# Optimization experiments

Measured on AMD Instinct MI355X. Metric: run time of the kernel, lower is better.

## Reference

```python
import jax, jax.numpy as jnp
import numpy as np

B, NQ, S, H, NH = 2, 1024, 4096, 1024, 16
HD = H // NH
EPS = 1e-6


def layer_norm(x, gamma, beta):
    mu = jnp.mean(x, axis=-1, keepdims=True)
    var = jnp.mean(jnp.square(x - mu), axis=-1, keepdims=True)
    return (x - mu) * jax.lax.rsqrt(var + EPS) * gamma + beta


def setup_inputs() -> dict:
    key = jax.random.key(0)
    ks = jax.random.split(key, 6)
    queries = jax.random.normal(ks[0], (B, NQ, H), dtype=jnp.float32)
    keys_values = jax.random.normal(ks[1], (B, S, H), dtype=jnp.float32)
    attention_mask = jax.random.uniform(ks[2], (B, S)) > 0.1
    attention_mask = attention_mask.at[:, 0].set(True)
    # params (torch Linear stored transposed here so y = x @ W + b)
    W_qkv = jax.random.normal(ks[3], (H, 3 * H), dtype=jnp.float32) * 0.02
    b_qkv = jnp.zeros((3 * H,), dtype=jnp.float32)
    W_out = jax.random.normal(ks[4], (H, H), dtype=jnp.float32) * 0.02
    b_out = jnp.zeros((H,), dtype=jnp.float32)
    gamma = jnp.ones((H,), dtype=jnp.float32)
    beta = jnp.zeros((H,), dtype=jnp.float32)
    return {"queries": queries, "keys_values": keys_values,
            "attention_mask": attention_mask,
            "W_qkv": W_qkv, "b_qkv": b_qkv, "W_out": W_out, "b_out": b_out,
            "gamma": gamma, "beta": beta}


def reference(queries, keys_values, attention_mask, W_qkv, b_qkv, W_out, b_out, gamma, beta):
    # shared LayerNorm + shared qkv projection applied to both streams
    q_in = layer_norm(queries, gamma, beta)
    kv_in = layer_norm(keys_values, gamma, beta)
    q = (q_in @ W_qkv + b_qkv)[..., :H]                    # [B,NQ,H]
    kv = kv_in @ W_qkv + b_qkv
    k = kv[..., H:2 * H]                                    # [B,S,H]
    v = kv[..., 2 * H:]                                     # [B,S,H]
    q = q.reshape(B, NQ, NH, HD)
    k = k.reshape(B, S, NH, HD)
    v = v.reshape(B, S, NH, HD)
    scale = 1.0 / np.sqrt(HD).astype(np.float32)
    scores = jnp.einsum('bqhd,bkhd->bhqk', q, k) * scale    # [B,NH,NQ,S]
    neg_inf = jnp.finfo(scores.dtype).min
    scores = jnp.where(attention_mask[:, None, None, :], scores, neg_inf)
    attn = jax.nn.softmax(scores, axis=-1)
    out = jnp.einsum('bhqk,bkhd->bqhd', attn, v).reshape(B, NQ, H)
    return out @ W_out + b_out
```

## Files before the change

### kernel.cpp

```cpp
#include <hip/hip_runtime.h>
#include <stdint.h>

#define DEVI __device__ __forceinline__

constexpr int Bb = 2, NQ = 1024, S = 4096, H = 1024, NH = 16, HD = 64;
constexpr int NSPLIT = 4, SLEN = S / NSPLIT;

typedef __bf16 bf16x8 __attribute__((ext_vector_type(8)));
typedef float f32x4 __attribute__((ext_vector_type(4)));
typedef int i32x4 __attribute__((ext_vector_type(4)));
typedef unsigned short u16;
typedef u16 u16x8 __attribute__((ext_vector_type(8)));

DEVI u16 f2bf(float f) {
  union { float f; unsigned u; } v; v.f = f;
  unsigned r = (v.u + 0x7fffu + ((v.u >> 16) & 1u)) >> 16;
  return (u16)r;
}

DEVI float bf2f(u16 x) {
  union { unsigned u; float f; } v; v.u = ((unsigned)x) << 16;
  return v.f;
}

DEVI float fexp2(float x) {
#if __has_builtin(__builtin_amdgcn_exp2f)
  return __builtin_amdgcn_exp2f(x);
#else
  return exp2f(x);
#endif
}

DEVI void gload_lds16(const void* g, void* lds) {
  __builtin_amdgcn_global_load_lds(
      (const __attribute__((address_space(1))) void*)(uintptr_t)g,
      (__attribute__((address_space(3))) void*)(uint32_t)(uintptr_t)lds,
      16, 0, 0);
}

DEVI void ln_body(const float* __restrict__ x, const float* __restrict__ gamma,
                  const float* __restrict__ beta, u16* __restrict__ out, int row) {
  int lane = threadIdx.x & 63;
  const float4* xr = (const float4*)(x + (size_t)row * H);
  float4 v[4];
  float s = 0.f, s2 = 0.f;
#pragma unroll
  for (int i = 0; i < 4; ++i) {
    v[i] = xr[lane + i * 64];
    s += v[i].x + v[i].y + v[i].z + v[i].w;
    s2 += v[i].x * v[i].x + v[i].y * v[i].y + v[i].z * v[i].z + v[i].w * v[i].w;
  }
#pragma unroll
  for (int d = 1; d < 64; d <<= 1) { s += __shfl_xor(s, d); s2 += __shfl_xor(s2, d); }
  float mu = s * (1.f / H);
  float rstd = rsqrtf(s2 * (1.f / H) - mu * mu + 1e-6f);
  u16* orow = out + (size_t)row * H;
  const float4* g4 = (const float4*)gamma;
  const float4* b4 = (const float4*)beta;
#pragma unroll
  for (int i = 0; i < 4; ++i) {
    float4 g = g4[lane + i * 64], bb = b4[lane + i * 64];
    ushort4 o;
    o.x = f2bf((v[i].x - mu) * rstd * g.x + bb.x);
    o.y = f2bf((v[i].y - mu) * rstd * g.y + bb.y);
    o.z = f2bf((v[i].z - mu) * rstd * g.z + bb.z);
    o.w = f2bf((v[i].w - mu) * rstd * g.w + bb.w);
    *(ushort4*)(orow + (size_t)(lane + i * 64) * 4) = o;
  }
}

__global__ __launch_bounds__(256) void prep_kernel(
    const unsigned char* __restrict__ mraw, unsigned char* __restrict__ maskN,
    const float* __restrict__ queries, const float* __restrict__ keys_values,
    const float* __restrict__ gamma, const float* __restrict__ beta,
    u16* __restrict__ Xq, u16* __restrict__ Xkv,
    const float* __restrict__ W_qkv, const float* __restrict__ W_out,
    u16* __restrict__ Wtq, u16* __restrict__ Wto) {
  __shared__ int isByte;
  __shared__ float tile[32][33];
  const int b = blockIdx.x;
  if (b == 0) {
    if (threadIdx.x == 0) isByte = 0;
    __syncthreads();
    int any = 0;
    for (int p = threadIdx.x; p < Bb * S; p += 256)
      if ((p & 3) && mraw[p]) any = 1;
    if (any) atomicOr(&isByte, 1);
    __syncthreads();
    const int bytemode = isByte;
    for (int i = threadIdx.x; i < Bb * S; i += 256) {
      unsigned char v = bytemode ? (unsigned char)(mraw[i] != 0)
                                 : (unsigned char)(((const int*)mraw)[i] != 0);
      maskN[i] = v;
    }
  } else if (b < 513) {
    ln_body(queries, gamma, beta, Xq, (b - 1) * 4 + (threadIdx.x >> 6));
  } else if (b < 2561) {
    ln_body(keys_values, gamma, beta, Xkv, (b - 513) * 4 + (threadIdx.x >> 6));
  } else {
    const float* in; u16* out; int C, t;
    if (b < 5633) { t = b - 2561; in = W_qkv; out = Wtq; C = 3 * H; }
    else          { t = b - 5633; in = W_out; out = Wto; C = H; }
    const int nbx = C / 32;
    int c0 = (t % nbx) * 32, r0 = (t / nbx) * 32;
    int tx = threadIdx.x & 31, ty = threadIdx.x >> 5;
#pragma unroll
    for (int i = 0; i < 32; i += 8)
      tile[ty + i][tx] = in[(size_t)(r0 + ty + i) * C + c0 + tx];
    __syncthreads();
#pragma unroll
    for (int i = 0; i < 32; i += 8)
      out[(size_t)(c0 + ty + i) * H + r0 + tx] = f2bf(tile[tx][ty + i]);
  }
}

#define GEMM_CORE(Ag, Bg)                                                        \
  f32x4 acc[4][4] = {};                                                          \
  {                                                                              \
    for (int k0 = 0; k0 < 1024; k0 += 32) {                                      \
      gload_lds16(Ag + (size_t)(c0 >> 2) * 1024 + k0 + (c0 & 3) * 8, Ash + c0 * 8); \
      gload_lds16(Ag + (size_t)(c1 >> 2) * 1024 + k0 + (c1 & 3) * 8, Ash + c1 * 8); \
      gload_lds16(Bg + (size_t)(c0 >> 2) * 1024 + k0 + (c0 & 3) * 8, Bsh + c0 * 8); \
      gload_lds16(Bg + (size_t)(c1 >> 2) * 1024 + k0 + (c1 & 3) * 8, Bsh + c1 * 8); \
      asm volatile("s_waitcnt vmcnt(0)" ::: "memory");                           \
      __syncthreads();                                                           \
      bf16x8 af[4], bfr[4];                                                      \
      _Pragma("unroll") for (int m = 0; m < 4; ++m)                              \
          af[m] = *(const bf16x8*)(Ash + (wr + m * 16 + fr) * 32 + fq * 8);      \
      _Pragma("unroll") for (int n = 0; n < 4; ++n)                              \
          bfr[n] = *(const bf16x8*)(Bsh + (wc + n * 16 + fr) * 32 + fq * 8);     \
      _Pragma("unroll") for (int m = 0; m < 4; ++m)                              \
          _Pragma("unroll") for (int n = 0; n < 4; ++n)                          \
              acc[m][n] = __builtin_amdgcn_mfma_f32_16x16x32_bf16(af[m], bfr[n], acc[m][n], 0, 0, 0); \
      __syncthreads();                                                           \
    }                                                                            \
  }

__global__ __launch_bounds__(512, 2) void gemm_kvq_kernel(
    const u16* __restrict__ Xkv, const u16* __restrict__ Xq,
    const u16* __restrict__ Wtq, const float* __restrict__ b_qkv,
    u16* __restrict__ KVbuf, u16* __restrict__ Qbuf) {
  __shared__ __align__(16) u16 Abuf[4][256 * 32];
  __shared__ __align__(16) u16 Bbuf[4][256 * 32];
  const int tid = threadIdx.x, wid = tid >> 6, lane = tid & 63;
  const int fr = lane & 15, fq = lane >> 4;
  const int wr = (wid >> 2) * 128, wc = (wid & 3) * 64;
  const int bid = blockIdx.x;
  const bool isQ = bid >= 256;
  int by, bx;
  const u16 *Ap, *Bp;
  const float* bias;
  if (!isQ) {
    const int xcd = bid & 7, loc = bid >> 3;
    by = xcd * 4 + (loc & 3); bx = loc >> 2;
    Ap = Xkv; Bp = Wtq + (size_t)H * H; bias = b_qkv + H;
  } else {
    const int t = bid - 256;
    by = t >> 2; bx = t & 3;
    Ap = Xq; Bp = Wtq; bias = b_qkv;
  }
  const u16* Ag = Ap + (size_t)(by * 256) * 1024;
  const u16* Bg = Bp + (size_t)(bx * 256) * 1024;

  f32x4 acc[8][4] = {};

  auto stage = [&](int tt) {
    const int k0 = tt * 32;
    u16* Ad = &Abuf[tt & 3][0];
    u16* Bd = &Bbuf[tt & 3][0];
#pragma unroll
    for (int l = 0; l < 2; ++l) {
      int ci = tid + l * 512;
      int row = ci >> 2, ch = ci & 3;
      int chs = ch ^ ((row >> 1) & 3);
      gload_lds16(Ag + (size_t)row * 1024 + k0 + chs * 8, Ad + ci * 8);
      gload_lds16(Bg + (size_t)row * 1024 + k0 + chs * 8, Bd + ci * 8);
    }
  };

#define KV_ITER(T, VM)                                                          \
  {                                                                             \
    asm volatile("s_waitcnt vmcnt(" #VM ")" ::: "memory");                      \
    __syncthreads();                                                            \
    const u16* Ac = &Abuf[(T) & 3][0];                                          \
    const u16* Bc = &Bbuf[(T) & 3][0];                                          \
    bf16x8 af[8], bfv[4];                                                       \
    _Pragma("unroll") for (int m = 0; m < 8; ++m) {                             \
      int row = wr + m * 16 + fr;                                               \
      af[m] = *(const bf16x8*)(Ac + row * 32 + (fq ^ ((row >> 1) & 3)) * 8);    \
    }                                                                           \
    _Pragma("unroll") for (int n = 0; n < 4; ++n) {                             \
      int row = wc + n * 16 + fr;                                               \
      bfv[n] = *(const bf16x8*)(Bc + row * 32 + (fq ^ ((row >> 1) & 3)) * 8);   \
    }                                                                           \
    if ((T) + 3 < 32) stage((T) + 3);                                           \
    __builtin_amdgcn_s_setprio(1);                                              \
    _Pragma("unroll") for (int m = 0; m < 8; ++m)                               \
      _Pragma("unroll") for (int n = 0; n < 4; ++n)                             \
        acc[m][n] = __builtin_amdgcn_mfma_f32_16x16x32_bf16(af[m], bfv[n], acc[m][n], 0, 0, 0); \
    __builtin_amdgcn_s_setprio(0);                                              \
  }

  stage(0);
  stage(1);
  stage(2);
  for (int t = 0; t < 29; ++t) KV_ITER(t, 8)
  KV_ITER(29, 8)
  KV_ITER(30, 4)
  KV_ITER(31, 0)
#undef KV_ITER

  constexpr float QSCALE = 0.125f * 1.4426950408889634f;
#pragma unroll
  for (int m = 0; m < 8; ++m)
#pragma unroll
    for (int n = 0; n < 4; ++n) {
      const int c = bx * 256 + wc + n * 16 + fr;
      const int r0 = by * 256 + wr + m * 16 + fq * 4;
      const float bv = bias[c];
      if (isQ) {
#pragma unroll
        for (int i = 0; i < 4; ++i) {
          int r = r0 + i;
          Qbuf[((((size_t)(r >> 10)) * NH + (c >> 6)) * NQ + (r & (NQ - 1))) * HD + (c & 63)] =
              f2bf((acc[m][n][i] + bv) * QSCALE);
        }
      } else if (c >= 1024) {
        int bb = r0 >> 12, kv = r0 & (S - 1);
        int cc = c - 1024, head = cc >> 6, d = cc & 63;
        ushort4 o;
        o.x = f2bf(acc[m][n][0] + bv);
        o.y = f2bf(acc[m][n][1] + bv);
        o.z = f2bf(acc[m][n][2] + bv);
        o.w = f2bf(acc[m][n][3] + bv);
        u16* vb = KVbuf + (size_t)Bb * NH * S * HD;
        *(ushort4*)(vb + (((size_t)(bb * NH + head)) * HD + d) * S + kv) = o;
      } else {
#pragma unroll
        for (int i = 0; i < 4; ++i) {
          int r = r0 + i;
          KVbuf[((((size_t)(r >> 12)) * NH + (c >> 6)) * S + (r & (S - 1))) * HD + (c & 63)] =
              f2bf(acc[m][n][i] + bv);
        }
      }
    }
}

__global__ __launch_bounds__(256) void gemm_out_kernel(
    const u16* __restrict__ A, const u16* __restrict__ Bt,
    const float* __restrict__ bias, float* __restrict__ outp) {
  __shared__ __align__(16) u16 Ash[128 * 32];
  __shared__ __align__(16) u16 Bsh[128 * 32];
  const int tid = threadIdx.x, w = tid >> 6, lane = tid & 63;
  const int c0 = tid, c1 = tid + 256;
  const int wr = (w >> 1) * 64, wc = (w & 1) * 64;
  const int fr = lane & 15, fq = lane >> 4;
  const int brow = blockIdx.y * 128, bcol = blockIdx.x * 128;
  const u16* Ag = A + (size_t)brow * 1024;
  const u16* Bg = Bt + (size_t)bcol * 1024;
  GEMM_CORE(Ag, Bg)
#pragma unroll
  for (int m = 0; m < 4; ++m)
#pragma unroll
    for (int n = 0; n < 4; ++n) {
      const int c = bcol + wc + n * 16 + fr;
      const int r0 = brow + wr + m * 16 + fq * 4;
#pragma unroll
      for (int i = 0; i < 4; ++i)
        outp[(size_t)(r0 + i) * H + c] = acc[m][n][i] + bias[c];
    }
}

__global__ __launch_bounds__(512, 4) void attn_kernel(
    const u16* __restrict__ Qb, const u16* __restrict__ Kb,
    const u16* __restrict__ Vt, const unsigned char* __restrict__ mask,
    u16* __restrict__ Opart, float2* __restrict__ ml) {
  __shared__ __align__(16) char smem[66560];
  u16* Ktile = (u16*)smem;
  u16* Vtile = (u16*)(smem + 32768);
  float* Mb = (float*)(smem + 65536);
  const int bflat = blockIdx.x;
  const int r = bflat & 7, idx = bflat >> 3;
  const int q0 = (idx & 3) * 256;
  const int g = (idx >> 2) * 8 + r;
  const int bh = g & 31, z = g >> 5;
  const int b = bh >> 4, kv0 = z * SLEN;
  const int tid = threadIdx.x, w = tid >> 6, lane = tid & 63;
  const int fr = lane & 15, fq = lane >> 4, fr7 = fr & 7;
  const u16* QgA = Qb + ((size_t)bh * NQ + q0 + w * 32) * HD;
  const u16* QgB = QgA + 16 * HD;
  const u16* Kg = Kb + (size_t)bh * S * HD;
  const u16* Vg = Vt + (size_t)bh * HD * S;
  const unsigned char* mg = mask + (size_t)b * S + kv0;

  const int kr0 = tid >> 3, kc0 = (tid & 7) ^ (kr0 & 7);
  const int kr1 = (tid + 512) >> 3, kc1 = ((tid + 512) & 7) ^ (kr1 & 7);
  const int vr0 = tid >> 4, vc0 = (tid & 15) ^ (vr0 & 15);
  const int vr1 = (tid + 512) >> 4, vc1 = ((tid + 512) & 15) ^ (vr1 & 15);

  bf16x8 qfA0 = *(const bf16x8*)(QgA + fr * HD + fq * 8);
  bf16x8 qfA1 = *(const bf16x8*)(QgA + fr * HD + 32 + fq * 8);
  bf16x8 qfB0 = *(const bf16x8*)(QgB + fr * HD + fq * 8);
  bf16x8 qfB1 = *(const bf16x8*)(QgB + fr * HD + 32 + fq * 8);

  const int A0 = ((((fq << 1)) & 3) * 16 + fr) << 2;
  const int A1 = ((((fq << 1) + 1) & 3) * 16 + fr) << 2;
  const bool lofq = (fq < 2);

  f32x4 oaccA[4] = {}, oaccB[4] = {};
  float mrowA = -1e30f, lrowA = 0.f, mrowB = -1e30f, lrowB = 0.f;

  auto stageKV = [&](int buf, int kts) {
    gload_lds16(Kg + (size_t)(kv0 + kts + kr0) * HD + kc0 * 8, Ktile + buf * 8192 + tid * 8);
    gload_lds16(Kg + (size_t)(kv0 + kts + kr1) * HD + kc1 * 8, Ktile + buf * 8192 + (tid + 512) * 8);
    gload_lds16(Vg + (size_t)vr0 * S + kv0 + kts + vc0 * 8, Vtile + buf * 8192 + tid * 8);
    gload_lds16(Vg + (size_t)vr1 * S + kv0 + kts + vc1 * 8, Vtile + buf * 8192 + (tid + 512) * 8);
  };

  auto process = [&](int cur, int h) {
    const u16* Kc = Ktile + cur * 8192 + h * 4096;
    const u16* Vc = Vtile + cur * 8192;
    const float* Mc = Mb + cur * 128 + h * 64;

    float svA[4][4], svB[4][4];
    __builtin_amdgcn_s_setprio(1);
#pragma unroll
    for (int nt = 0; nt < 4; ++nt) {
      const u16* kb2 = Kc + (nt * 16 + fr) * 64;
      bf16x8 k0v = *(const bf16x8*)(kb2 + ((fq) ^ fr7) * 8);
      bf16x8 k1v = *(const bf16x8*)(kb2 + ((4 + fq) ^ fr7) * 8);
      f32x4 tA = {}, tB = {};
      tA = __builtin_amdgcn_mfma_f32_16x16x32_bf16(k0v, qfA0, tA, 0, 0, 0);
      tA = __builtin_amdgcn_mfma_f32_16x16x32_bf16(k1v, qfA1, tA, 0, 0, 0);
      tB = __builtin_amdgcn_mfma_f32_16x16x32_bf16(k0v, qfB0, tB, 0, 0, 0);
      tB = __builtin_amdgcn_mfma_f32_16x16x32_bf16(k1v, qfB1, tB, 0, 0, 0);
      float4 mb = *(const float4*)&Mc[nt * 16 + fq * 4];
      svA[nt][0] = tA[0] + mb.x; svA[nt][1] = tA[1] + mb.y;
      svA[nt][2] = tA[2] + mb.z; svA[nt][3] = tA[3] + mb.w;
      svB[nt][0] = tB[0] + mb.x; svB[nt][1] = tB[1] + mb.y;
      svB[nt][2] = tB[2] + mb.z; svB[nt][3] = tB[3] + mb.w;
    }
    __builtin_amdgcn_s_setprio(0);

    float pmaxA, pmaxB;
    {
      float a0 = fmaxf(fmaxf(svA[0][0], svA[0][1]), fmaxf(svA[0][2], svA[0][3]));
      float a1 = fmaxf(fmaxf(svA[1][0], svA[1][1]), fmaxf(svA[1][2], svA[1][3]));
      float a2 = fmaxf(fmaxf(svA[2][0], svA[2][1]), fmaxf(svA[2][2], svA[2][3]));
      float a3 = fmaxf(fmaxf(svA[3][0], svA[3][1]), fmaxf(svA[3][2], svA[3][3]));
      pmaxA = fmaxf(fmaxf(a0, a1), fmaxf(a2, a3));
      float b0 = fmaxf(fmaxf(svB[0][0], svB[0][1]), fmaxf(svB[0][2], svB[0][3]));
      float b1 = fmaxf(fmaxf(svB[1][0], svB[1][1]), fmaxf(svB[1][2], svB[1][3]));
      float b2 = fmaxf(fmaxf(svB[2][0], svB[2][1]), fmaxf(svB[2][2], svB[2][3]));
      float b3 = fmaxf(fmaxf(svB[3][0], svB[3][1]), fmaxf(svB[3][2], svB[3][3]));
      pmaxB = fmaxf(fmaxf(b0, b1), fmaxf(b2, b3));
    }
    if (__any(pmaxA > mrowA + 12.f)) {
      pmaxA = fmaxf(pmaxA, __shfl_xor(pmaxA, 16));
      pmaxA = fmaxf(pmaxA, __shfl_xor(pmaxA, 32));
      float nm = fmaxf(mrowA, pmaxA);
      float al = fexp2(mrowA - nm);
      mrowA = nm; lrowA *= al;
#pragma unroll
      for (int nt = 0; nt < 4; ++nt)
#pragma unroll
        for (int i = 0; i < 4; ++i) oaccA[nt][i] *= al;
    }
    if (__any(pmaxB > mrowB + 12.f)) {
      pmaxB = fmaxf(pmaxB, __shfl_xor(pmaxB, 16));
      pmaxB = fmaxf(pmaxB, __shfl_xor(pmaxB, 32));
      float nm = fmaxf(mrowB, pmaxB);
      float al = fexp2(mrowB - nm);
      mrowB = nm; lrowB *= al;
#pragma unroll
      for (int nt = 0; nt < 4; ++nt)
#pragma unroll
        for (int i = 0; i < 4; ++i) oaccB[nt][i] *= al;
    }

    float pA[4][4], pB[4][4];
#pragma unroll
    for (int nt = 0; nt < 4; ++nt)
#pragma unroll
      for (int i = 0; i < 4; ++i) {
        pA[nt][i] = fexp2(svA[nt][i] - mrowA);
        pB[nt][i] = fexp2(svB[nt][i] - mrowB);
      }
    {
      float s0 = (pA[0][0] + pA[0][1]) + (pA[0][2] + pA[0][3]);
      float s1 = (pA[1][0] + pA[1][1]) + (pA[1][2] + pA[1][3]);
      float s2 = (pA[2][0] + pA[2][1]) + (pA[2][2] + pA[2][3]);
      float s3 = (pA[3][0] + pA[3][1]) + (pA[3][2] + pA[3][3]);
      lrowA += (s0 + s1) + (s2 + s3);
      float t0 = (pB[0][0] + pB[0][1]) + (pB[0][2] + pB[0][3]);
      float t1 = (pB[1][0] + pB[1][1]) + (pB[1][2] + pB[1][3]);
      float t2 = (pB[2][0] + pB[2][1]) + (pB[2][2] + pB[2][3]);
      float t3 = (pB[3][0] + pB[3][1]) + (pB[3][2] + pB[3][3]);
      lrowB += (t0 + t1) + (t2 + t3);
    }

    int pkA[4][2], pkB[4][2];
#pragma unroll
    for (int nt = 0; nt < 4; ++nt) {
      asm("v_cvt_pk_bf16_f32 %0, %1, %2" : "=v"(pkA[nt][0]) : "v"(pA[nt][0]), "v"(pA[nt][1]));
      asm("v_cvt_pk_bf16_f32 %0, %1, %2" : "=v"(pkA[nt][1]) : "v"(pA[nt][2]), "v"(pA[nt][3]));
      asm("v_cvt_pk_bf16_f32 %0, %1, %2" : "=v"(pkB[nt][0]) : "v"(pB[nt][0]), "v"(pB[nt][1]));
      asm("v_cvt_pk_bf16_f32 %0, %1, %2" : "=v"(pkB[nt][1]) : "v"(pB[nt][2]), "v"(pB[nt][3]));
    }

#pragma unroll
    for (int b2 = 0; b2 < 2; ++b2) {
      i32x4 wvA, wvB;
      {
        int w0a = __builtin_amdgcn_ds_bpermute(A0, pkA[2 * b2][0]);
        int w0b = __builtin_amdgcn_ds_bpermute(A0, pkA[2 * b2 + 1][0]);
        int w1a = __builtin_amdgcn_ds_bpermute(A0, pkA[2 * b2][1]);
        int w1b = __builtin_amdgcn_ds_bpermute(A0, pkA[2 * b2 + 1][1]);
        int w2a = __builtin_amdgcn_ds_bpermute(A1, pkA[2 * b2][0]);
        int w2b = __builtin_amdgcn_ds_bpermute(A1, pkA[2 * b2 + 1][0]);
        int w3a = __builtin_amdgcn_ds_bpermute(A1, pkA[2 * b2][1]);
        int w3b = __builtin_amdgcn_ds_bpermute(A1, pkA[2 * b2 + 1][1]);
        wvA[0] = lofq ? w0a : w0b;
        wvA[1] = lofq ? w1a : w1b;
        wvA[2] = lofq ? w2a : w2b;
        wvA[3] = lofq ? w3a : w3b;
      }
      {
        int w0a = __builtin_amdgcn_ds_bpermute(A0, pkB[2 * b2][0]);
        int w0b = __builtin_amdgcn_ds_bpermute(A0, pkB[2 * b2 + 1][0]);
        int w1a = __builtin_amdgcn_ds_bpermute(A0, pkB[2 * b2][1]);
        int w1b = __builtin_amdgcn_ds_bpermute(A0, pkB[2 * b2 + 1][1]);
        int w2a = __builtin_amdgcn_ds_bpermute(A1, pkB[2 * b2][0]);
        int w2b = __builtin_amdgcn_ds_bpermute(A1, pkB[2 * b2 + 1][0]);
        int w3a = __builtin_amdgcn_ds_bpermute(A1, pkB[2 * b2][1]);
        int w3b = __builtin_amdgcn_ds_bpermute(A1, pkB[2 * b2 + 1][1]);
        wvB[0] = lofq ? w0a : w0b;
        wvB[1] = lofq ? w1a : w1b;
        wvB[2] = lofq ? w2a : w2b;
        wvB[3] = lofq ? w3a : w3b;
      }
      bf16x8 pfragA = __builtin_bit_cast(bf16x8, wvA);
      bf16x8 pfragB = __builtin_bit_cast(bf16x8, wvB);
      __builtin_amdgcn_s_setprio(1);
#pragma unroll
      for (int nt = 0; nt < 4; ++nt) {
        const u16* vb2 = Vc + (nt * 16 + fr) * 128;
        bf16x8 vf = *(const bf16x8*)(vb2 + ((h * 8 + b2 * 4 + fq) ^ fr) * 8);
        oaccA[nt] = __builtin_amdgcn_mfma_f32_16x16x32_bf16(vf, pfragA, oaccA[nt], 0, 0, 0);
        oaccB[nt] = __builtin_amdgcn_mfma_f32_16x16x32_bf16(vf, pfragB, oaccB[nt], 0, 0, 0);
      }
      __builtin_amdgcn_s_setprio(0);
    }
  };

  if (tid < 128) Mb[tid] = mg[tid] ? 0.f : -1e30f;
  stageKV(0, 0);
  asm volatile("s_waitcnt vmcnt(0)" ::: "memory");
  __syncthreads();

  int cur = 0;
  for (int kt = 0; kt < SLEN; kt += 128) {
    const int nb = cur ^ 1, kn = kt + 128;
    if (kn < SLEN) {
      if (tid < 128) Mb[nb * 128 + tid] = mg[kn + tid] ? 0.f : -1e30f;
      stageKV(nb, kn);
    }
    process(cur, 0);
    process(cur, 1);
    asm volatile("s_waitcnt vmcnt(0)" ::: "memory");
    __syncthreads();
    cur = nb;
  }

  lrowA += __shfl_xor(lrowA, 16);
  lrowA += __shfl_xor(lrowA, 32);
  lrowB += __shfl_xor(lrowB, 16);
  lrowB += __shfl_xor(lrowB, 32);
  if (fq == 0) {
    ml[((size_t)z * 32 + bh) * NQ + q0 + w * 32 + fr] = float2{mrowA, lrowA};
    ml[((size_t)z * 32 + bh) * NQ + q0 + w * 32 + 16 + fr] = float2{mrowB, lrowB};
  }

  float* tb = (float*)smem + w * 1088;
  const int qloc = lane >> 2, dl = lane & 3;
#pragma unroll
  for (int gsel = 0; gsel < 2; ++gsel) {
    const f32x4* oc = gsel ? oaccB : oaccA;
#pragma unroll
    for (int nt = 0; nt < 4; ++nt)
#pragma unroll
      for (int i = 0; i < 4; ++i)
        tb[fr * 68 + nt * 16 + fq * 4 + i] = oc[nt][i];
    const float* trow = tb + qloc * 68 + dl * 16;
    u16* gdst = Opart +
        (((size_t)z * 32 + bh) * NQ + q0 + w * 32 + gsel * 16 + qloc) * 64 + dl * 16;
    u16x8 o0, o1;
#pragma unroll
    for (int j = 0; j < 8; ++j) {
      o0[j] = f2bf(trow[j]);
      o1[j] = f2bf(trow[8 + j]);
    }
    *(u16x8*)gdst = o0;
    *(u16x8*)(gdst + 8) = o1;
  }
}

__global__ __launch_bounds__(256) void combine_kernel(
    const u16* __restrict__ Opart, const float2* __restrict__ ml,
    u16* __restrict__ out) {
  const int bh = blockIdx.y, b = bh >> 4, h = bh & 15;
  const int q = blockIdx.x * 64 + (threadIdx.x >> 2);
  const int dl = threadIdx.x & 3;
  float2 mm[NSPLIT];
  float M = -1e30f;
#pragma unroll
  for (int zz = 0; zz < NSPLIT; ++zz) {
    mm[zz] = ml[((size_t)zz * 32 + bh) * NQ + q];
    M = fmaxf(M, mm[zz].x);
  }
  float wz[NSPLIT], lsum = 0.f;
#pragma unroll
  for (int zz = 0; zz < NSPLIT; ++zz) {
    wz[zz] = fexp2(mm[zz].x - M);
    lsum += mm[zz].y * wz[zz];
  }
  const float inv = 1.f / lsum;
  float acc[16] = {};
#pragma unroll
  for (int zz = 0; zz < NSPLIT; ++zz) {
    const u16* op = Opart + (((size_t)zz * 32 + bh) * NQ + q) * 64 + dl * 16;
    u16x8 a0 = *(const u16x8*)op;
    u16x8 a1 = *(const u16x8*)(op + 8);
    float wi = wz[zz] * inv;
#pragma unroll
    for (int j = 0; j < 8; ++j) {
      acc[j] += wi * bf2f(a0[j]);
      acc[8 + j] += wi * bf2f(a1[j]);
    }
  }
  u16* orow = out + ((size_t)b * NQ + q) * H + h * HD + dl * 16;
  u16x8 o0, o1;
#pragma unroll
  for (int j = 0; j < 8; ++j) {
    o0[j] = f2bf(acc[j]);
    o1[j] = f2bf(acc[8 + j]);
  }
  *(u16x8*)orow = o0;
  *(u16x8*)(orow + 8) = o1;
}

extern "C" void kernel_launch(void* const* d_in, const int* in_sizes, int n_in,
                              void* d_out, int out_size, void* d_ws, size_t ws_size,
                              hipStream_t stream) {
  const float* queries = (const float*)d_in[0];
  const float* keys_values = (const float*)d_in[1];
  const void* amask = d_in[2];
  const float* W_qkv = (const float*)d_in[3];
  const float* b_qkv = (const float*)d_in[4];
  const float* W_out = (const float*)d_in[5];
  const float* b_out = (const float*)d_in[6];
  const float* gamma = (const float*)d_in[7];
  const float* beta = (const float*)d_in[8];

  char* ws = (char*)d_ws;
  unsigned char* maskN = (unsigned char*)ws;
  u16* Xq = (u16*)(ws + 8192);
  u16* Xkv = Xq + (size_t)Bb * NQ * H;
  u16* Wtq = Xkv + (size_t)Bb * S * H;
  u16* Wto = Wtq + (size_t)3 * H * H;
  u16* Qbuf = Wto + (size_t)H * H;
  u16* Kbuf = Qbuf + (size_t)Bb * NQ * H;
  u16* Aout = Kbuf + (size_t)2 * Bb * S * H;
  u16* Opart = (u16*)(ws + 8192);
  float2* ml = (float2*)((char*)Opart + (size_t)NSPLIT * 32 * NQ * 64 * 2);

  hipLaunchKernelGGL(prep_kernel, dim3(6657), dim3(256), 0, stream,
                     (const unsigned char*)amask, maskN, queries, keys_values,
                     gamma, beta, Xq, Xkv, W_qkv, W_out, Wtq, Wto);
  hipLaunchKernelGGL(gemm_kvq_kernel, dim3(288), dim3(512), 0, stream,
                     Xkv, Xq, Wtq, b_qkv, Kbuf, Qbuf);
  hipLaunchKernelGGL(attn_kernel, dim3(NQ / 256 * Bb * NH * NSPLIT), dim3(512), 0, stream,
                     Qbuf, Kbuf, Kbuf + (size_t)Bb * S * H, maskN, Opart, ml);
  hipLaunchKernelGGL(combine_kernel, dim3(NQ / 64, Bb * NH), dim3(256), 0, stream,
                     Opart, ml, Aout);
  hipLaunchKernelGGL(gemm_out_kernel, dim3(H / 128, Bb * NQ / 128), dim3(256), 0, stream,
                     Aout, Wto, b_out, (float*)d_out);
}
```

Measured before the change: 185.1 us.

## Pipeline out-proj GEMM with 4-stage LDS ring and shrink attention KV tile

The output-projection GEMM now uses a 4-buffer LDS ring that prefetches three k-steps ahead, with swizzled LDS addressing and raised MFMA priority, replacing the load-wait-compute macro. This is meant to hide global load latency that the old scheme exposed at every step. Separately, the attention kernel shrinks its KV tile from 128 to 64 keys. That roughly halves shared memory per block and allows more resident blocks, at the cost of twice as many loop iterations and barriers.

New measurement: 169.6 us. 1.09x faster.

```diff
diff --git a/kernel.cpp b/kernel.cpp
--- a/kernel.cpp
+++ b/kernel.cpp
@@ -114,28 +114,6 @@
   }
 }
 
-#define GEMM_CORE(Ag, Bg)                                                        \
-  f32x4 acc[4][4] = {};                                                          \
-  {                                                                              \
-    for (int k0 = 0; k0 < 1024; k0 += 32) {                                      \
-      gload_lds16(Ag + (size_t)(c0 >> 2) * 1024 + k0 + (c0 & 3) * 8, Ash + c0 * 8); \
-      gload_lds16(Ag + (size_t)(c1 >> 2) * 1024 + k0 + (c1 & 3) * 8, Ash + c1 * 8); \
-      gload_lds16(Bg + (size_t)(c0 >> 2) * 1024 + k0 + (c0 & 3) * 8, Bsh + c0 * 8); \
-      gload_lds16(Bg + (size_t)(c1 >> 2) * 1024 + k0 + (c1 & 3) * 8, Bsh + c1 * 8); \
-      asm volatile("s_waitcnt vmcnt(0)" ::: "memory");                           \
-      __syncthreads();                                                           \
-      bf16x8 af[4], bfr[4];                                                      \
-      _Pragma("unroll") for (int m = 0; m < 4; ++m)                              \
-          af[m] = *(const bf16x8*)(Ash + (wr + m * 16 + fr) * 32 + fq * 8);      \
-      _Pragma("unroll") for (int n = 0; n < 4; ++n)                              \
-          bfr[n] = *(const bf16x8*)(Bsh + (wc + n * 16 + fr) * 32 + fq * 8);     \
-      _Pragma("unroll") for (int m = 0; m < 4; ++m)                              \
-          _Pragma("unroll") for (int n = 0; n < 4; ++n)                          \
-              acc[m][n] = __builtin_amdgcn_mfma_f32_16x16x32_bf16(af[m], bfr[n], acc[m][n], 0, 0, 0); \
-      __syncthreads();                                                           \
-    }                                                                            \
-  }
-
 __global__ __launch_bounds__(512, 2) void gemm_kvq_kernel(
     const u16* __restrict__ Xkv, const u16* __restrict__ Xq,
     const u16* __restrict__ Wtq, const float* __restrict__ b_qkv,
@@ -246,19 +224,66 @@
     }
 }
 
-__global__ __launch_bounds__(256) void gemm_out_kernel(
+__global__ __launch_bounds__(256, 2) void gemm_out_kernel(
     const u16* __restrict__ A, const u16* __restrict__ Bt,
     const float* __restrict__ bias, float* __restrict__ outp) {
-  __shared__ __align__(16) u16 Ash[128 * 32];
-  __shared__ __align__(16) u16 Bsh[128 * 32];
-  const int tid = threadIdx.x, w = tid >> 6, lane = tid & 63;
-  const int c0 = tid, c1 = tid + 256;
-  const int wr = (w >> 1) * 64, wc = (w & 1) * 64;
+  __shared__ __align__(16) u16 Abuf[4][128 * 32];
+  __shared__ __align__(16) u16 Bbuf[4][128 * 32];
+  const int tid = threadIdx.x, wid = tid >> 6, lane = tid & 63;
   const int fr = lane & 15, fq = lane >> 4;
+  const int wr = (wid >> 1) * 64, wc = (wid & 1) * 64;
   const int brow = blockIdx.y * 128, bcol = blockIdx.x * 128;
   const u16* Ag = A + (size_t)brow * 1024;
   const u16* Bg = Bt + (size_t)bcol * 1024;
-  GEMM_CORE(Ag, Bg)
+
+  f32x4 acc[4][4] = {};
+
+  auto stage = [&](int tt) {
+    const int k0 = tt * 32;
+    u16* Ad = &Abuf[tt & 3][0];
+    u16* Bd = &Bbuf[tt & 3][0];
+#pragma unroll
+    for (int l = 0; l < 2; ++l) {
+      int ci = tid + l * 256;
+      int row = ci >> 2, ch = ci & 3;
+      int chs = ch ^ ((row >> 1) & 3);
+      gload_lds16(Ag + (size_t)row * 1024 + k0 + chs * 8, Ad + ci * 8);
+      gload_lds16(Bg + (size_t)row * 1024 + k0 + chs * 8, Bd + ci * 8);
+    }
+  };
+
+#define OUT_ITER(T, VM)                                                         \
+  {                                                                             \
+    asm volatile("s_waitcnt vmcnt(" #VM ")" ::: "memory");                      \
+    __syncthreads();                                                            \
+    const u16* Ac = &Abuf[(T) & 3][0];                                          \
+    const u16* Bc = &Bbuf[(T) & 3][0];                                          \
+    bf16x8 af[4], bfv[4];                                                       \
+    _Pragma("unroll") for (int m = 0; m < 4; ++m) {                             \
+      int row = wr + m * 16 + fr;                                               \
+      af[m] = *(const bf16x8*)(Ac + row * 32 + (fq ^ ((row >> 1) & 3)) * 8);    \
+    }                                                                           \
+    _Pragma("unroll") for (int n = 0; n < 4; ++n) {                             \
+      int row = wc + n * 16 + fr;                                               \
+      bfv[n] = *(const bf16x8*)(Bc + row * 32 + (fq ^ ((row >> 1) & 3)) * 8);   \
+    }                                                                           \
+    if ((T) + 3 < 32) stage((T) + 3);                                           \
+    __builtin_amdgcn_s_setprio(1);                                              \
+    _Pragma("unroll") for (int m = 0; m < 4; ++m)                               \
+      _Pragma("unroll") for (int n = 0; n < 4; ++n)                             \
+        acc[m][n] = __builtin_amdgcn_mfma_f32_16x16x32_bf16(af[m], bfv[n], acc[m][n], 0, 0, 0); \
+    __builtin_amdgcn_s_setprio(0);                                              \
+  }
+
+  stage(0);
+  stage(1);
+  stage(2);
+  for (int t = 0; t < 29; ++t) OUT_ITER(t, 8)
+  OUT_ITER(29, 8)
+  OUT_ITER(30, 4)
+  OUT_ITER(31, 0)
+#undef OUT_ITER
+
 #pragma unroll
   for (int m = 0; m < 4; ++m)
 #pragma unroll
@@ -275,10 +300,10 @@
     const u16* __restrict__ Qb, const u16* __restrict__ Kb,
     const u16* __restrict__ Vt, const unsigned char* __restrict__ mask,
     u16* __restrict__ Opart, float2* __restrict__ ml) {
-  __shared__ __align__(16) char smem[66560];
+  __shared__ __align__(16) char smem[34816];
   u16* Ktile = (u16*)smem;
-  u16* Vtile = (u16*)(smem + 32768);
-  float* Mb = (float*)(smem + 65536);
+  u16* Vtile = Ktile + 8192;
+  float* Mb = (float*)(Vtile + 8192);
   const int bflat = blockIdx.x;
   const int r = bflat & 7, idx = bflat >> 3;
   const int q0 = (idx & 3) * 256;
@@ -293,10 +318,7 @@
   const u16* Vg = Vt + (size_t)bh * HD * S;
   const unsigned char* mg = mask + (size_t)b * S + kv0;
 
-  const int kr0 = tid >> 3, kc0 = (tid & 7) ^ (kr0 & 7);
-  const int kr1 = (tid + 512) >> 3, kc1 = ((tid + 512) & 7) ^ (kr1 & 7);
-  const int vr0 = tid >> 4, vc0 = (tid & 15) ^ (vr0 & 15);
-  const int vr1 = (tid + 512) >> 4, vc1 = ((tid + 512) & 15) ^ (vr1 & 15);
+  const int rs = tid >> 3, gs = (tid & 7) ^ (rs & 7);
 
   bf16x8 qfA0 = *(const bf16x8*)(QgA + fr * HD + fq * 8);
   bf16x8 qfA1 = *(const bf16x8*)(QgA + fr * HD + 32 + fq * 8);
@@ -310,17 +332,23 @@
   f32x4 oaccA[4] = {}, oaccB[4] = {};
   float mrowA = -1e30f, lrowA = 0.f, mrowB = -1e30f, lrowB = 0.f;
 
-  auto stageKV = [&](int buf, int kts) {
-    gload_lds16(Kg + (size_t)(kv0 + kts + kr0) * HD + kc0 * 8, Ktile + buf * 8192 + tid * 8);
-    gload_lds16(Kg + (size_t)(kv0 + kts + kr1) * HD + kc1 * 8, Ktile + buf * 8192 + (tid + 512) * 8);
-    gload_lds16(Vg + (size_t)vr0 * S + kv0 + kts + vc0 * 8, Vtile + buf * 8192 + tid * 8);
-    gload_lds16(Vg + (size_t)vr1 * S + kv0 + kts + vc1 * 8, Vtile + buf * 8192 + (tid + 512) * 8);
-  };
-
-  auto process = [&](int cur, int h) {
-    const u16* Kc = Ktile + cur * 8192 + h * 4096;
-    const u16* Vc = Vtile + cur * 8192;
-    const float* Mc = Mb + cur * 128 + h * 64;
+  if (tid < 64) Mb[tid] = mg[tid] ? 0.f : -1e30f;
+  gload_lds16(Kg + (size_t)(kv0 + rs) * HD + gs * 8, Ktile + tid * 8);
+  gload_lds16(Vg + (size_t)rs * S + kv0 + gs * 8, Vtile + tid * 8);
+  asm volatile("s_waitcnt vmcnt(0)" ::: "memory");
+  __syncthreads();
+
+  int cur = 0;
+  for (int kt = 0; kt < SLEN; kt += 64) {
+    const int nb = cur ^ 1, kn = kt + 64;
+    if (kn < SLEN) {
+      if (tid < 64) Mb[nb * 64 + tid] = mg[kn + tid] ? 0.f : -1e30f;
+      gload_lds16(Kg + (size_t)(kv0 + kn + rs) * HD + gs * 8, Ktile + nb * 4096 + tid * 8);
+      gload_lds16(Vg + (size_t)rs * S + kv0 + kn + gs * 8, Vtile + nb * 4096 + tid * 8);
+    }
+
+    const u16* Kc = Ktile + cur * 4096;
+    const u16* Vc = Vtile + cur * 4096;
 
     float svA[4][4], svB[4][4];
     __builtin_amdgcn_s_setprio(1);
@@ -334,7 +362,7 @@
       tA = __builtin_amdgcn_mfma_f32_16x16x32_bf16(k1v, qfA1, tA, 0, 0, 0);
       tB = __builtin_amdgcn_mfma_f32_16x16x32_bf16(k0v, qfB0, tB, 0, 0, 0);
       tB = __builtin_amdgcn_mfma_f32_16x16x32_bf16(k1v, qfB1, tB, 0, 0, 0);
-      float4 mb = *(const float4*)&Mc[nt * 16 + fq * 4];
+      float4 mb = *(const float4*)&Mb[cur * 64 + nt * 16 + fq * 4];
       svA[nt][0] = tA[0] + mb.x; svA[nt][1] = tA[1] + mb.y;
       svA[nt][2] = tA[2] + mb.z; svA[nt][3] = tA[3] + mb.w;
       svB[nt][0] = tB[0] + mb.x; svB[nt][1] = tB[1] + mb.y;
@@ -444,29 +472,14 @@
       __builtin_amdgcn_s_setprio(1);
 #pragma unroll
       for (int nt = 0; nt < 4; ++nt) {
-        const u16* vb2 = Vc + (nt * 16 + fr) * 128;
-        bf16x8 vf = *(const bf16x8*)(vb2 + ((h * 8 + b2 * 4 + fq) ^ fr) * 8);
+        const u16* vb2 = Vc + (nt * 16 + fr) * 64;
+        bf16x8 vf = *(const bf16x8*)(vb2 + ((b2 * 4 + fq) ^ fr7) * 8);
         oaccA[nt] = __builtin_amdgcn_mfma_f32_16x16x32_bf16(vf, pfragA, oaccA[nt], 0, 0, 0);
         oaccB[nt] = __builtin_amdgcn_mfma_f32_16x16x32_bf16(vf, pfragB, oaccB[nt], 0, 0, 0);
       }
       __builtin_amdgcn_s_setprio(0);
     }
-  };
-
-  if (tid < 128) Mb[tid] = mg[tid] ? 0.f : -1e30f;
-  stageKV(0, 0);
-  asm volatile("s_waitcnt vmcnt(0)" ::: "memory");
-  __syncthreads();
-
-  int cur = 0;
-  for (int kt = 0; kt < SLEN; kt += 128) {
-    const int nb = cur ^ 1, kn = kt + 128;
-    if (kn < SLEN) {
-      if (tid < 128) Mb[nb * 128 + tid] = mg[kn + tid] ? 0.f : -1e30f;
-      stageKV(nb, kn);
-    }
-    process(cur, 0);
-    process(cur, 1);
+
     asm volatile("s_waitcnt vmcnt(0)" ::: "memory");
     __syncthreads();
     cur = nb;
```
